# Kernel optimization log

Measured on AMD Instinct MI355X. Metric: run time of the kernel, lower is better.

## Reference

```python
import jax, jax.numpy as jnp
import numpy as np

T, HID, H, HKV, D = 4096, 2048, 16, 2, 128
EPS = 1e-6


def setup_inputs() -> dict:
    key = jax.random.key(0)
    ks = jax.random.split(key, 5)
    hidden_states = jax.random.normal(ks[0], (T, HID), dtype=jnp.float32)
    # rope angles: build realistic cos/sin from positions and inv-freqs
    inv_freq = 1.0 / (10000.0 ** (jnp.arange(0, D, 2, dtype=jnp.float32) / D))
    ang = jnp.arange(T, dtype=jnp.float32)[:, None] * inv_freq[None, :]  # [T, D/2]
    ang = jnp.concatenate([ang, ang], axis=-1)  # [T, D]
    cos, sin = jnp.cos(ang), jnp.sin(ang)
    w_qkv = jax.random.normal(ks[1], (HID, (2 * H + 2 * HKV) * D), dtype=jnp.float32) * (HID ** -0.5)
    w_o = jax.random.normal(ks[2], (H * D, HID), dtype=jnp.float32) * ((H * D) ** -0.5)
    q_norm_w = jnp.ones((D,), dtype=jnp.float32)
    k_norm_w = jnp.ones((D,), dtype=jnp.float32)
    return {"hidden_states": hidden_states, "cos": cos, "sin": sin,
            "w_qkv": w_qkv, "w_o": w_o, "q_norm_w": q_norm_w, "k_norm_w": k_norm_w}


def _rms_norm(x, w):
    var = jnp.mean(x * x, axis=-1, keepdims=True)
    return x * jax.lax.rsqrt(var + EPS) * w


def _rotate_half(x):
    x1, x2 = x[..., : D // 2], x[..., D // 2:]
    return jnp.concatenate([-x2, x1], axis=-1)


def _rope(x, cos, sin):
    # x: [T, h, D]; cos/sin: [T, D]
    return x * cos[:, None, :] + _rotate_half(x) * sin[:, None, :]


def reference(hidden_states, cos, sin, w_qkv, w_o, q_norm_w, k_norm_w):
    qkv = hidden_states @ w_qkv  # [T, (2H+2HKV)*D]
    q_sz, kv_sz = 2 * H * D, HKV * D
    # packed query+gate: view as [T, H, 2D], first half query, second half gate
    qg = qkv[:, :q_sz].reshape(T, H, 2 * D)
    q, gate = qg[..., :D], qg[..., D:]
    k = qkv[:, q_sz:q_sz + kv_sz].reshape(T, HKV, D)
    v = qkv[:, q_sz + kv_sz:].reshape(T, HKV, D)
    q = _rms_norm(q, q_norm_w)
    k = _rms_norm(k, k_norm_w)
    q = _rope(q, cos, sin)
    k = _rope(k, cos, sin)
    # GQA: expand kv heads to H
    rep = H // HKV
    k = jnp.repeat(k, rep, axis=1)  # [T, H, D]
    v = jnp.repeat(v, rep, axis=1)
    scale = D ** -0.5
    scores = jnp.einsum('thd,shd->hts', q, k) * scale  # [H, T, T]
    causal = jnp.tril(jnp.ones((T, T), dtype=bool))
    scores = jnp.where(causal[None], scores, jnp.finfo(scores.dtype).min)
    probs = jax.nn.softmax(scores, axis=-1)
    attn = jnp.einsum('hts,shd->thd', probs, v)  # [T, H, D]
    out = attn.reshape(T, H * D) * jax.nn.sigmoid(gate.reshape(T, H * D))
    return out @ w_o
```

## Files before the change

### kernel.cpp

```cpp
#include <hip/hip_runtime.h>
#include <hip/hip_bf16.h>
#include <math.h>


namespace {
constexpr int kT   = 4096;
constexpr int kHid = 2048;
constexpr int kH   = 16;
constexpr int kHkv = 2;
constexpr int kD   = 128;
constexpr int kNqkv = (2 * kH + 2 * kHkv) * kD;
constexpr int kQsz  = 2 * kH * kD;
constexpr int kRowU = kNqkv * 2;
constexpr float kEps = 1e-6f;
constexpr float kScale = 0.08838834764831845f;
}

typedef __attribute__((ext_vector_type(8))) short short8;
typedef __attribute__((ext_vector_type(4))) float floatx4;

__device__ inline unsigned short f2bf(float x) {
  unsigned u = __float_as_uint(x);
  u = (u + 0x7fffu + ((u >> 16) & 1u)) >> 16;
  return (unsigned short)u;
}

__device__ inline void gload_lds16(const void* g, void* l) {
  typedef const __attribute__((address_space(1))) unsigned GQ;
  typedef __attribute__((address_space(3))) unsigned LQ;
  __builtin_amdgcn_global_load_lds((GQ*)g, (LQ*)l, 16, 0, 0);
}

__global__ __launch_bounds__(256)
void cvt_bf16(const float* __restrict__ in, unsigned short* __restrict__ out,
              long nelem) {
  long i = ((long)blockIdx.x * 256 + threadIdx.x) * 4;
  if (i >= nelem) return;
  float4 v = *(const float4*)(in + i);
  unsigned long long p = (unsigned long long)f2bf(v.x) |
                         ((unsigned long long)f2bf(v.y) << 16) |
                         ((unsigned long long)f2bf(v.z) << 32) |
                         ((unsigned long long)f2bf(v.w) << 48);
  *(unsigned long long*)(out + i) = p;
}

__global__ __launch_bounds__(256)
void transpose_cvt(const float* __restrict__ in, unsigned short* __restrict__ out,
                   int R, int C) {
  __shared__ float t[32][33];
  const int bx = blockIdx.x * 32;
  const int by = blockIdx.y * 32;
  const int x = threadIdx.x & 31, y = threadIdx.x >> 5;
#pragma unroll
  for (int j = 0; j < 4; ++j)
    t[y * 4 + j][x] = in[(long)(by + y * 4 + j) * C + bx + x];
  __syncthreads();
#pragma unroll
  for (int j = 0; j < 4; ++j)
    out[(long)(bx + y * 4 + j) * R + by + x] = f2bf(t[x][y * 4 + j]);
}

__global__ __launch_bounds__(256)
void vt_transpose(const float* __restrict__ qkv, unsigned short* __restrict__ VtG) {
  __shared__ float t[32][33];
  const int t0 = blockIdx.x * 32;
  const int c0 = blockIdx.y * 32;
  const int x = threadIdx.x & 31, y = threadIdx.x >> 5;
#pragma unroll
  for (int j = 0; j < 4; ++j)
    t[y * 4 + j][x] = qkv[(long)(t0 + y * 4 + j) * kNqkv + 4352 + c0 + x];
  __syncthreads();
#pragma unroll
  for (int j = 0; j < 4; ++j)
    VtG[(long)(c0 + y * 4 + j) * kT + t0 + x] = f2bf(t[x][y * 4 + j]);
}

__global__ __launch_bounds__(256)
void gemm_bf16(const unsigned short* __restrict__ A,
               const unsigned short* __restrict__ Bt, float* __restrict__ C,
               int M, int N, int K) {
  __shared__ __align__(16) unsigned short As[128 * 64];
  __shared__ __align__(16) unsigned short Bs[128 * 64];
  const int tid = threadIdx.x;
  const int lane = tid & 63;
  const int w = tid >> 6;
  const int wr = w >> 1, wc = w & 1;
  const int n = lane & 15;
  const int quad = lane >> 4;
  const long bm = (long)blockIdx.x * 128, bn = (long)blockIdx.y * 128;

  floatx4 acc[4][4];
  floatx4 zero = {0.f, 0.f, 0.f, 0.f};
#pragma unroll
  for (int a = 0; a < 4; ++a)
#pragma unroll
    for (int b = 0; b < 4; ++b) acc[a][b] = zero;

  for (int k0 = 0; k0 < K; k0 += 64) {
    __syncthreads();
#pragma unroll
    for (int it = 0; it < 4; ++it) {
      int ci = it * 256 + tid;
      int r = ci >> 3, c = ci & 7;
      int cg = c ^ (r & 7);
      gload_lds16(A + (bm + r) * (long)K + k0 + cg * 8, As + (it * 256 + w * 64) * 8);
      gload_lds16(Bt + (bn + r) * (long)K + k0 + cg * 8, Bs + (it * 256 + w * 64) * 8);
    }
    __syncthreads();

#pragma unroll
    for (int ks = 0; ks < 2; ++ks) {
      short8 af[4], bf[4];
#pragma unroll
      for (int a = 0; a < 4; ++a) {
        int m = wr * 64 + a * 16 + n;
        af[a] = *(const short8*)(As + m * 64 + ((4 * ks + quad) ^ (m & 7)) * 8);
      }
#pragma unroll
      for (int b = 0; b < 4; ++b) {
        int nn = wc * 64 + b * 16 + n;
        bf[b] = *(const short8*)(Bs + nn * 64 + ((4 * ks + quad) ^ (nn & 7)) * 8);
      }
#pragma unroll
      for (int a = 0; a < 4; ++a)
#pragma unroll
        for (int b = 0; b < 4; ++b)
          acc[a][b] = __builtin_amdgcn_mfma_f32_16x16x32_bf16(af[a], bf[b], acc[a][b], 0, 0, 0);
    }
  }
#pragma unroll
  for (int a = 0; a < 4; ++a)
#pragma unroll
    for (int b = 0; b < 4; ++b)
#pragma unroll
      for (int r = 0; r < 4; ++r)
        C[(bm + wr * 64 + a * 16 + quad * 4 + r) * (long)N + bn + wc * 64 + b * 16 + n] =
            acc[a][b][r];
}

__global__ __launch_bounds__(128)
void norm_rope_cvt(float* qkv, const float* __restrict__ cosb,
                   const float* __restrict__ sinb, const float* __restrict__ qw,
                   const float* __restrict__ kw) {
  unsigned short* qkvu = (unsigned short*)qkv;
  const int blk = blockIdx.x;
  const int t = blk / 18;
  const int h = blk % 18;
  const int i = threadIdx.x;

  const bool isq = (h < kH);
  const long base = (long)t * kNqkv + (isq ? h * 2 * kD : kQsz + (h - kH) * kD);
  float x = qkv[base + i];
  float v = x * x;
#pragma unroll
  for (int off = 1; off < 64; off <<= 1) v += __shfl_xor(v, off, 64);
  __shared__ float wsum[2];
  if ((i & 63) == 0) wsum[i >> 6] = v;
  __syncthreads();
  float rms = rsqrtf((wsum[0] + wsum[1]) * (1.0f / kD) + kEps);
  float nv = x * rms * (isq ? qw[i] : kw[i]);
  __shared__ float nb[128];
  nb[i] = nv;
  __syncthreads();
  float rot = (i < 64) ? -nb[i + 64] : nb[i - 64];
  float ro = nv * cosb[t * kD + i] + rot * sinb[t * kD + i];
  if (isq) {
    float g = qkv[base + kD + i];
    qkv[base + kD + i] = 1.0f / (1.0f + __expf(-g));
    qkvu[(long)t * kRowU + 512 * h + i] = f2bf(ro);
  } else {
    qkvu[(long)t * kRowU + 8192 + 256 * (h - kH) + i] = f2bf(ro);
  }
}

__global__ __launch_bounds__(256)
void flash_attn_mfma(const unsigned short* qkvu, const float* qkvf,
                     const unsigned short* VtG, unsigned short* __restrict__ og) {
  __shared__ __align__(16) unsigned short Ks[2][64 * 128];
  __shared__ __align__(16) unsigned short Vt[2][128 * 64];

  const int tid = threadIdx.x;
  const int lane = tid & 63;
  const int w = tid >> 6;
  const int n = lane & 15;
  const int quad = lane >> 4;
  const int g = blockIdx.x;
  const int h = g & 15;
  const int gi = g >> 4;
  const int bm = (gi < 16) ? (31 - gi) : (gi - 16);
  const int hk = h >> 3;
  const int q0 = bm * 128;

  short8 qf[2][4];
#pragma unroll
  for (int mt = 0; mt < 2; ++mt) {
    const unsigned short* qrow =
        qkvu + (long)(q0 + 32 * w + 16 * mt + n) * kRowU + 512 * h;
#pragma unroll
    for (int ks = 0; ks < 4; ++ks)
      qf[mt][ks] = *(const short8*)(qrow + 32 * ks + 8 * quad);
  }
  short8 lfrag;
  {
    short o = (n == 0) ? (short)0x3F80 : (short)0;
    lfrag = (short8){o, o, o, o, o, o, o, o};
  }

  floatx4 O[2][8];
  floatx4 Ol[2];
  floatx4 zero = {0.f, 0.f, 0.f, 0.f};
#pragma unroll
  for (int mt = 0; mt < 2; ++mt) {
    Ol[mt] = zero;
#pragma unroll
    for (int dt = 0; dt < 8; ++dt) O[mt][dt] = zero;
  }

  auto stage = [&](int b, int kn) {
#pragma unroll
    for (int it = 0; it < 4; ++it) {
      int pc = (w * 4 + it) * 64 + lane;
      int r = pc >> 4, c = pc & 15;
      int lc = c ^ (r & 15);
      gload_lds16(qkvu + (long)(kn * 64 + r) * kRowU + 8192 + 256 * hk + 8 * lc,
                  &Ks[b][(w * 4 + it) * 512]);
    }
#pragma unroll
    for (int it = 0; it < 4; ++it) {
      int pc = (w * 4 + it) * 64 + lane;
      int d = pc >> 3, c = pc & 7;
      int lc = c ^ (d & 7);
      gload_lds16(VtG + (long)hk * (128 * kT) + (long)d * kT + kn * 64 + 8 * lc,
                  &Vt[b][(w * 4 + it) * 512]);
    }
  };

  const int kn_end = 2 * bm + 1;
  stage(0, 0);

  for (int kn = 0; kn <= kn_end; ++kn) {
    const int cur = kn & 1;
    if (kn < kn_end) {
      stage(cur ^ 1, kn + 1);
      __asm__ volatile("s_waitcnt vmcnt(8)" ::: "memory");
    } else {
      __asm__ volatile("s_waitcnt vmcnt(0)" ::: "memory");
    }
    __builtin_amdgcn_s_barrier();
    __builtin_amdgcn_sched_barrier(0);

    const unsigned short* Kc = Ks[cur];
    const unsigned short* Vc = Vt[cur];

    floatx4 S[2][4];
#pragma unroll
    for (int mt = 0; mt < 2; ++mt)
#pragma unroll
      for (int ct = 0; ct < 4; ++ct) S[mt][ct] = zero;
    __builtin_amdgcn_s_setprio(1);
#pragma unroll
    for (int ks = 0; ks < 4; ++ks) {
#pragma unroll
      for (int ct = 0; ct < 4; ++ct) {
        int row = 16 * ct + n;
        short8 kf = *(const short8*)(Kc + row * 128 + ((4 * ks + quad) ^ n) * 8);
        S[0][ct] = __builtin_amdgcn_mfma_f32_16x16x32_bf16(qf[0][ks], kf, S[0][ct], 0, 0, 0);
        S[1][ct] = __builtin_amdgcn_mfma_f32_16x16x32_bf16(qf[1][ks], kf, S[1][ct], 0, 0, 0);
      }
    }
    __builtin_amdgcn_s_setprio(0);
    __asm__ volatile("s_waitcnt lgkmcnt(0)" ::: "memory");
    __builtin_amdgcn_s_barrier();
    __builtin_amdgcn_sched_barrier(0);

    unsigned short* Ps = (unsigned short*)Kc;
    const bool needmask = (kn >= 2 * bm);
    const int jbase = (kn - 2 * bm) * 64;
    const int hi = n >> 3, lo = n & 7;
#pragma unroll
    for (int mt = 0; mt < 2; ++mt) {
#pragma unroll
      for (int r = 0; r < 4; ++r) {
        int prow = 32 * w + 16 * mt + quad * 4 + r;
        float p0 = __expf(S[mt][0][r] * kScale);
        float p1 = __expf(S[mt][1][r] * kScale);
        float p2 = __expf(S[mt][2][r] * kScale);
        float p3 = __expf(S[mt][3][r] * kScale);
        if (needmask) {
          if (jbase + n > prow) p0 = 0.f;
          if (jbase + 16 + n > prow) p1 = 0.f;
          if (jbase + 32 + n > prow) p2 = 0.f;
          if (jbase + 48 + n > prow) p3 = 0.f;
        }
        int sw = prow & 7;
        Ps[prow * 64 + (((0 + hi) ^ sw) << 3) + lo] = f2bf(p0);
        Ps[prow * 64 + (((2 + hi) ^ sw) << 3) + lo] = f2bf(p1);
        Ps[prow * 64 + (((4 + hi) ^ sw) << 3) + lo] = f2bf(p2);
        Ps[prow * 64 + (((6 + hi) ^ sw) << 3) + lo] = f2bf(p3);
      }
    }
    __asm__ volatile("s_waitcnt lgkmcnt(0)" ::: "memory");
    __builtin_amdgcn_sched_barrier(0);

    __builtin_amdgcn_s_setprio(1);
#pragma unroll
    for (int ks = 0; ks < 2; ++ks) {
      int r0 = 32 * w + n, r1 = 32 * w + 16 + n;
      short8 pf0 = *(const short8*)(Ps + r0 * 64 + (((4 * ks + quad) ^ (r0 & 7)) << 3));
      short8 pf1 = *(const short8*)(Ps + r1 * 64 + (((4 * ks + quad) ^ (r1 & 7)) << 3));
      Ol[0] = __builtin_amdgcn_mfma_f32_16x16x32_bf16(pf0, lfrag, Ol[0], 0, 0, 0);
      Ol[1] = __builtin_amdgcn_mfma_f32_16x16x32_bf16(pf1, lfrag, Ol[1], 0, 0, 0);
#pragma unroll
      for (int dt = 0; dt < 8; ++dt) {
        int d = 16 * dt + n;
        short8 vf = *(const short8*)(Vc + d * 64 + (((4 * ks + quad) ^ (d & 7)) << 3));
        O[0][dt] = __builtin_amdgcn_mfma_f32_16x16x32_bf16(pf0, vf, O[0][dt], 0, 0, 0);
        O[1][dt] = __builtin_amdgcn_mfma_f32_16x16x32_bf16(pf1, vf, O[1][dt], 0, 0, 0);
      }
    }
    __builtin_amdgcn_s_setprio(0);
    __asm__ volatile("s_waitcnt lgkmcnt(0)" ::: "memory");
    __builtin_amdgcn_s_barrier();
    __builtin_amdgcn_sched_barrier(0);
  }

#pragma unroll
  for (int mt = 0; mt < 2; ++mt) {
#pragma unroll
    for (int r = 0; r < 4; ++r) {
      float l = __shfl(Ol[mt][r], quad << 4, 64);
      float inv = 1.0f / l;
      int row = q0 + 32 * w + 16 * mt + quad * 4 + r;
#pragma unroll
      for (int dt = 0; dt < 8; ++dt) {
        int col = 16 * dt + n;
        float gte = qkvf[(long)row * kNqkv + 256 * h + 128 + col];
        og[(long)row * kHid + 128 * h + col] = f2bf(O[mt][dt][r] * inv * gte);
      }
    }
  }
}

extern "C" void kernel_launch(void* const* d_in, const int* in_sizes, int n_in,
                              void* d_out, int out_size, void* d_ws, size_t ws_size,
                              hipStream_t stream) {
  (void)in_sizes; (void)n_in; (void)out_size; (void)ws_size;
  const float* hs   = (const float*)d_in[0];
  const float* cosb = (const float*)d_in[1];
  const float* sinb = (const float*)d_in[2];
  const float* wqkv = (const float*)d_in[3];
  const float* wo   = (const float*)d_in[4];
  const float* qw   = (const float*)d_in[5];
  const float* kw   = (const float*)d_in[6];
  float* out = (float*)d_out;

  char* ws = (char*)d_ws;
  float* qkv = (float*)ws;
  unsigned short* hsb = (unsigned short*)(ws + 75497472);
  unsigned short* og  = hsb;
  unsigned short* wt  = (unsigned short*)(ws + 92274688);
  unsigned short* VtG = wt;

  cvt_bf16<<<dim3(8192), 256, 0, stream>>>(hs, hsb, (long)kT * kHid);
  transpose_cvt<<<dim3(kNqkv / 32, kHid / 32), 256, 0, stream>>>(wqkv, wt, kHid, kNqkv);
  gemm_bf16<<<dim3(kT / 128, kNqkv / 128), 256, 0, stream>>>(hsb, wt, qkv, kT, kNqkv, kHid);
  vt_transpose<<<dim3(kT / 32, 8), 256, 0, stream>>>(qkv, VtG);
  norm_rope_cvt<<<dim3(kT * 18), 128, 0, stream>>>(qkv, cosb, sinb, qw, kw);
  flash_attn_mfma<<<dim3(kT / 128 * kH), 256, 0, stream>>>((const unsigned short*)qkv, qkv, VtG, og);
  transpose_cvt<<<dim3(kHid / 32, kHid / 32), 256, 0, stream>>>(wo, wt, kHid, kHid);
  gemm_bf16<<<dim3(kT / 128, kHid / 128), 256, 0, stream>>>(og, wt, out, kT, kHid, kHid);
}
```

Before: 554.7 us.

## Enlarge flash-attention query tile to 256 rows with a dedicated P buffer

Each attention block now processes 256 query rows, with four 16-row m-tiles per wave, instead of 128. This reuses every staged K/V tile across twice as many queries. P now goes to its own region of dynamic shared memory instead of overwriting the K buffer, which lets the barrier between the QK^T step and the P writes be dropped. The setprio and sched_barrier hints and the heavy-first block ordering are also removed. The risks are fewer blocks (256) with strongly uneven causal work, one block per CU, and higher register pressure.

Result: slower. 570.6 us (+2.9%).

```diff
diff --git a/kernel.cpp b/kernel.cpp
--- a/kernel.cpp
+++ b/kernel.cpp
@@ -173,11 +173,13 @@
   }
 }
 
-__global__ __launch_bounds__(256)
+__global__ __launch_bounds__(256, 1)
 void flash_attn_mfma(const unsigned short* qkvu, const float* qkvf,
                      const unsigned short* VtG, unsigned short* __restrict__ og) {
-  __shared__ __align__(16) unsigned short Ks[2][64 * 128];
-  __shared__ __align__(16) unsigned short Vt[2][128 * 64];
+  extern __shared__ __align__(16) unsigned short smem[];
+  unsigned short* KsB = smem;
+  unsigned short* VtB = smem + 16384;
+  unsigned short* Ps  = smem + 32768;
 
   const int tid = threadIdx.x;
   const int lane = tid & 63;
@@ -186,16 +188,15 @@
   const int quad = lane >> 4;
   const int g = blockIdx.x;
   const int h = g & 15;
-  const int gi = g >> 4;
-  const int bm = (gi < 16) ? (31 - gi) : (gi - 16);
+  const int bm = g >> 4;
   const int hk = h >> 3;
-  const int q0 = bm * 128;
-
-  short8 qf[2][4];
-#pragma unroll
-  for (int mt = 0; mt < 2; ++mt) {
+  const int q0 = bm * 256;
+
+  short8 qf[4][4];
+#pragma unroll
+  for (int mt = 0; mt < 4; ++mt) {
     const unsigned short* qrow =
-        qkvu + (long)(q0 + 32 * w + 16 * mt + n) * kRowU + 512 * h;
+        qkvu + (long)(q0 + 64 * w + 16 * mt + n) * kRowU + 512 * h;
 #pragma unroll
     for (int ks = 0; ks < 4; ++ks)
       qf[mt][ks] = *(const short8*)(qrow + 32 * ks + 8 * quad);
@@ -206,24 +207,26 @@
     lfrag = (short8){o, o, o, o, o, o, o, o};
   }
 
-  floatx4 O[2][8];
-  floatx4 Ol[2];
+  floatx4 O[4][8];
+  floatx4 Ol[4];
   floatx4 zero = {0.f, 0.f, 0.f, 0.f};
 #pragma unroll
-  for (int mt = 0; mt < 2; ++mt) {
+  for (int mt = 0; mt < 4; ++mt) {
     Ol[mt] = zero;
 #pragma unroll
     for (int dt = 0; dt < 8; ++dt) O[mt][dt] = zero;
   }
 
   auto stage = [&](int b, int kn) {
+    unsigned short* Kd = KsB + b * 8192;
+    unsigned short* Vd = VtB + b * 8192;
 #pragma unroll
     for (int it = 0; it < 4; ++it) {
       int pc = (w * 4 + it) * 64 + lane;
       int r = pc >> 4, c = pc & 15;
       int lc = c ^ (r & 15);
       gload_lds16(qkvu + (long)(kn * 64 + r) * kRowU + 8192 + 256 * hk + 8 * lc,
-                  &Ks[b][(w * 4 + it) * 512]);
+                  Kd + (w * 4 + it) * 512);
     }
 #pragma unroll
     for (int it = 0; it < 4; ++it) {
@@ -231,11 +234,11 @@
       int d = pc >> 3, c = pc & 7;
       int lc = c ^ (d & 7);
       gload_lds16(VtG + (long)hk * (128 * kT) + (long)d * kT + kn * 64 + 8 * lc,
-                  &Vt[b][(w * 4 + it) * 512]);
+                  Vd + (w * 4 + it) * 512);
     }
   };
 
-  const int kn_end = 2 * bm + 1;
+  const int kn_end = 4 * bm + 3;
   stage(0, 0);
 
   for (int kn = 0; kn <= kn_end; ++kn) {
@@ -247,41 +250,35 @@
       __asm__ volatile("s_waitcnt vmcnt(0)" ::: "memory");
     }
     __builtin_amdgcn_s_barrier();
-    __builtin_amdgcn_sched_barrier(0);
-
-    const unsigned short* Kc = Ks[cur];
-    const unsigned short* Vc = Vt[cur];
-
-    floatx4 S[2][4];
-#pragma unroll
-    for (int mt = 0; mt < 2; ++mt)
+
+    const unsigned short* Kc = KsB + cur * 8192;
+    const unsigned short* Vc = VtB + cur * 8192;
+
+    floatx4 S[4][4];
+#pragma unroll
+    for (int mt = 0; mt < 4; ++mt)
 #pragma unroll
       for (int ct = 0; ct < 4; ++ct) S[mt][ct] = zero;
-    __builtin_amdgcn_s_setprio(1);
 #pragma unroll
     for (int ks = 0; ks < 4; ++ks) {
 #pragma unroll
       for (int ct = 0; ct < 4; ++ct) {
         int row = 16 * ct + n;
         short8 kf = *(const short8*)(Kc + row * 128 + ((4 * ks + quad) ^ n) * 8);
-        S[0][ct] = __builtin_amdgcn_mfma_f32_16x16x32_bf16(qf[0][ks], kf, S[0][ct], 0, 0, 0);
-        S[1][ct] = __builtin_amdgcn_mfma_f32_16x16x32_bf16(qf[1][ks], kf, S[1][ct], 0, 0, 0);
-      }
-    }
-    __builtin_amdgcn_s_setprio(0);
-    __asm__ volatile("s_waitcnt lgkmcnt(0)" ::: "memory");
-    __builtin_amdgcn_s_barrier();
-    __builtin_amdgcn_sched_barrier(0);
-
-    unsigned short* Ps = (unsigned short*)Kc;
-    const bool needmask = (kn >= 2 * bm);
-    const int jbase = (kn - 2 * bm) * 64;
+#pragma unroll
+        for (int mt = 0; mt < 4; ++mt)
+          S[mt][ct] = __builtin_amdgcn_mfma_f32_16x16x32_bf16(qf[mt][ks], kf, S[mt][ct], 0, 0, 0);
+      }
+    }
+
+    const bool needmask = (kn >= 4 * bm);
+    const int jbase = (kn - 4 * bm) * 64;
     const int hi = n >> 3, lo = n & 7;
 #pragma unroll
-    for (int mt = 0; mt < 2; ++mt) {
+    for (int mt = 0; mt < 4; ++mt) {
 #pragma unroll
       for (int r = 0; r < 4; ++r) {
-        int prow = 32 * w + 16 * mt + quad * 4 + r;
+        int prow = 64 * w + 16 * mt + quad * 4 + r;
         float p0 = __expf(S[mt][0][r] * kScale);
         float p1 = __expf(S[mt][1][r] * kScale);
         float p2 = __expf(S[mt][2][r] * kScale);
@@ -300,37 +297,36 @@
       }
     }
     __asm__ volatile("s_waitcnt lgkmcnt(0)" ::: "memory");
-    __builtin_amdgcn_sched_barrier(0);
-
-    __builtin_amdgcn_s_setprio(1);
+
 #pragma unroll
     for (int ks = 0; ks < 2; ++ks) {
-      int r0 = 32 * w + n, r1 = 32 * w + 16 + n;
-      short8 pf0 = *(const short8*)(Ps + r0 * 64 + (((4 * ks + quad) ^ (r0 & 7)) << 3));
-      short8 pf1 = *(const short8*)(Ps + r1 * 64 + (((4 * ks + quad) ^ (r1 & 7)) << 3));
-      Ol[0] = __builtin_amdgcn_mfma_f32_16x16x32_bf16(pf0, lfrag, Ol[0], 0, 0, 0);
-      Ol[1] = __builtin_amdgcn_mfma_f32_16x16x32_bf16(pf1, lfrag, Ol[1], 0, 0, 0);
+      short8 pf[4];
+#pragma unroll
+      for (int mt = 0; mt < 4; ++mt) {
+        int r0 = 64 * w + 16 * mt + n;
+        pf[mt] = *(const short8*)(Ps + r0 * 64 + (((4 * ks + quad) ^ (r0 & 7)) << 3));
+        Ol[mt] = __builtin_amdgcn_mfma_f32_16x16x32_bf16(pf[mt], lfrag, Ol[mt], 0, 0, 0);
+      }
 #pragma unroll
       for (int dt = 0; dt < 8; ++dt) {
         int d = 16 * dt + n;
         short8 vf = *(const short8*)(Vc + d * 64 + (((4 * ks + quad) ^ (d & 7)) << 3));
-        O[0][dt] = __builtin_amdgcn_mfma_f32_16x16x32_bf16(pf0, vf, O[0][dt], 0, 0, 0);
-        O[1][dt] = __builtin_amdgcn_mfma_f32_16x16x32_bf16(pf1, vf, O[1][dt], 0, 0, 0);
-      }
-    }
-    __builtin_amdgcn_s_setprio(0);
+#pragma unroll
+        for (int mt = 0; mt < 4; ++mt)
+          O[mt][dt] = __builtin_amdgcn_mfma_f32_16x16x32_bf16(pf[mt], vf, O[mt][dt], 0, 0, 0);
+      }
+    }
     __asm__ volatile("s_waitcnt lgkmcnt(0)" ::: "memory");
     __builtin_amdgcn_s_barrier();
-    __builtin_amdgcn_sched_barrier(0);
-  }
-
-#pragma unroll
-  for (int mt = 0; mt < 2; ++mt) {
+  }
+
+#pragma unroll
+  for (int mt = 0; mt < 4; ++mt) {
 #pragma unroll
     for (int r = 0; r < 4; ++r) {
       float l = __shfl(Ol[mt][r], quad << 4, 64);
       float inv = 1.0f / l;
-      int row = q0 + 32 * w + 16 * mt + quad * 4 + r;
+      int row = q0 + 64 * w + 16 * mt + quad * 4 + r;
 #pragma unroll
       for (int dt = 0; dt < 8; ++dt) {
         int col = 16 * dt + n;
@@ -366,7 +362,7 @@
   gemm_bf16<<<dim3(kT / 128, kNqkv / 128), 256, 0, stream>>>(hsb, wt, qkv, kT, kNqkv, kHid);
   vt_transpose<<<dim3(kT / 32, 8), 256, 0, stream>>>(qkv, VtG);
   norm_rope_cvt<<<dim3(kT * 18), 128, 0, stream>>>(qkv, cosb, sinb, qw, kw);
-  flash_attn_mfma<<<dim3(kT / 128 * kH), 256, 0, stream>>>((const unsigned short*)qkv, qkv, VtG, og);
+  flash_attn_mfma<<<dim3(kT / 256 * kH), 256, 98304, stream>>>((const unsigned short*)qkv, qkv, VtG, og);
   transpose_cvt<<<dim3(kHid / 32, kHid / 32), 256, 0, stream>>>(wo, wt, kHid, kHid);
   gemm_bf16<<<dim3(kT / 128, kHid / 128), 256, 0, stream>>>(og, wt, out, kT, kHid, kHid);
 }
```
